# Kernel tuning notes

Measured on AMD Instinct MI355X. Metric: run time of the kernel, lower is better.

## Reference

```python
import jax, jax.numpy as jnp
import numpy as np

N, E = 50000, 400000
C_IN, C_OUT = 64, 32
K = 9  # kernel_size 3x3


def _quad_basis(t):
    # open B-spline basis, degree 2, per torch_spline_conv: k_mod in {0,1,2}
    # t = frac(pseudo * (kernel_size - degree)) = pseudo here (kernel_size=3, degree=2)
    return jnp.stack([0.5 * (1.0 - t) ** 2, -t * t + t + 0.5, 0.5 * t * t], axis=-1)  # [E,3]


def spline_basis(pseudo):
    # kernel_size=[3,3], degree=2, open spline: v = p*(3-2)=p, floor(v)=0 for p in [0,1),
    # so weight index for combination s is exactly s = k_mod0 + 3*k_mod1.
    q0 = _quad_basis(pseudo[:, 0])  # [E,3] varies with s%3
    q1 = _quad_basis(pseudo[:, 1])  # [E,3] varies with s//3
    return (q1[:, :, None] * q0[:, None, :]).reshape(-1, K)  # [E,9]


def spline_conv(x, src, dst, B, W, root, bias, n_nodes):
    xj = x[src]  # gather source node features [E,Cin]
    msg = jnp.zeros((xj.shape[0], W.shape[-1]), x.dtype)
    for k in range(K):  # fixed small kernel loop; avoids [E,K,Cin] blowup
        msg = msg + (xj * B[:, k, None]) @ W[k]
    agg = jax.ops.segment_sum(msg, dst, num_segments=n_nodes)  # aggr='add'
    return agg + x @ root + bias


def setup_inputs() -> dict:
    key = jax.random.key(0)
    ks = jax.random.split(key, 10)
    x = jax.random.normal(ks[0], (N, C_IN), jnp.float32)
    edge_index = jax.random.randint(ks[1], (2, E), 0, N, jnp.int64)
    pseudo = jax.random.uniform(ks[2], (E, 2), jnp.float32)
    skip = jax.random.normal(ks[3], (N, C_OUT), jnp.float32)
    s1 = 1.0 / np.sqrt(C_IN)
    s2 = 1.0 / np.sqrt(C_OUT)
    W1 = jax.random.normal(ks[4], (K, C_IN, C_OUT), jnp.float32) * s1
    root1 = jax.random.normal(ks[5], (C_IN, C_OUT), jnp.float32) * s1
    b1 = jnp.zeros((C_OUT,), jnp.float32)
    W2 = jax.random.normal(ks[6], (K, C_OUT, C_OUT), jnp.float32) * s2
    root2 = jax.random.normal(ks[7], (C_OUT, C_OUT), jnp.float32) * s2
    b2 = jnp.zeros((C_OUT,), jnp.float32)
    return {"x": x, "edge_index": edge_index, "pseudo": pseudo, "skip": skip,
            "W1": W1, "root1": root1, "b1": b1, "W2": W2, "root2": root2, "b2": b2}


def reference(x, edge_index, pseudo, skip, W1, root1, b1, W2, root2, b2):
    src, dst = edge_index[0], edge_index[1]  # flow: source_to_target
    B = spline_basis(pseudo)  # [E,9]
    n = x.shape[0]
    h = jax.nn.relu(spline_conv(x, src, dst, B, W1, root1, b1, n))
    h = jnp.concatenate([h, skip], axis=1)  # [N, Cout+Cskip] == [N, Cin]
    h = jax.nn.relu(spline_conv(h, src, dst, B, W1, root1, b1, n))
    h = jax.nn.relu(spline_conv(h, src, dst, B, W2, root2, b2, n))
    return h
```

## Files before the change

kernel.cpp:

```cpp
#include <hip/hip_runtime.h>
#include <hip/hip_bf16.h>


typedef __attribute__((ext_vector_type(8))) short short8;
typedef __attribute__((ext_vector_type(4))) float f32x4;

__device__ __forceinline__ float blo(unsigned u) {
    union { unsigned u; float f; } x; x.u = u << 16; return x.f;
}
__device__ __forceinline__ float bhi(unsigned u) {
    union { unsigned u; float f; } x; x.u = u & 0xffff0000u; return x.f;
}
__device__ __forceinline__ unsigned short f2bf(float f) {
    union { float f; unsigned u; } x; x.f = f;
    unsigned r = x.u + 0x7fffu + ((x.u >> 16) & 1u);
    return (unsigned short)(r >> 16);
}
__device__ __forceinline__ short8 cvt8(const float* p) {
    float4 a = *(const float4*)p;
    float4 b = *(const float4*)(p + 4);
    short8 r;
    r[0] = (short)f2bf(a.x); r[1] = (short)f2bf(a.y);
    r[2] = (short)f2bf(a.z); r[3] = (short)f2bf(a.w);
    r[4] = (short)f2bf(b.x); r[5] = (short)f2bf(b.y);
    r[6] = (short)f2bf(b.z); r[7] = (short)f2bf(b.w);
    return r;
}

#define YROW 296

__device__ __forceinline__ void m_phase(const unsigned short* sY,
                                        const int* __restrict__ sstart,
                                        const float4* __restrict__ erec,
                                        uint4* __restrict__ msgOut,
                                        int n0, int t, int N, int E)
{
    const int e0 = sstart[n0];
    const int e1 = (n0 + 32 < N) ? sstart[n0 + 32] : E;
    const int l  = t & 3;

    int e = e0 + (t >> 2);
    if (e >= e1) return;
    float4 r = erec[e];
    while (true) {
        const int en = e + 64;
        float4 rn;
        if (en < e1) rn = erec[en];

        const int srcl = __float_as_int(r.x) - n0;
        const int dp   = __float_as_int(r.y);
        const float p0 = r.z, p1 = r.w;

        const float qb[3] = {0.5f * (1.f - p0) * (1.f - p0), -p0 * p0 + p0 + 0.5f, 0.5f * p0 * p0};
        const float qa[3] = {0.5f * (1.f - p1) * (1.f - p1), -p1 * p1 + p1 + 0.5f, 0.5f * p1 * p1};

        const uint4* yb = (const uint4*)(sY + srcl * YROW) + l;
        float s[8] = {0.f, 0.f, 0.f, 0.f, 0.f, 0.f, 0.f, 0.f};
        #pragma unroll
        for (int a = 0; a < 3; ++a) {
            float z[8] = {0.f, 0.f, 0.f, 0.f, 0.f, 0.f, 0.f, 0.f};
            #pragma unroll
            for (int b = 0; b < 3; ++b) {
                uint4 v = yb[(a * 3 + b) * 4];
                const float cw = qb[b];
                z[0] = fmaf(cw, blo(v.x), z[0]); z[1] = fmaf(cw, bhi(v.x), z[1]);
                z[2] = fmaf(cw, blo(v.y), z[2]); z[3] = fmaf(cw, bhi(v.y), z[3]);
                z[4] = fmaf(cw, blo(v.z), z[4]); z[5] = fmaf(cw, bhi(v.z), z[5]);
                z[6] = fmaf(cw, blo(v.w), z[6]); z[7] = fmaf(cw, bhi(v.w), z[7]);
            }
            #pragma unroll
            for (int j = 0; j < 8; ++j) s[j] = fmaf(qa[a], z[j], s[j]);
        }

        union { uint4 u; __hip_bfloat162 h[4]; } o;
        #pragma unroll
        for (int j = 0; j < 4; ++j)
            o.h[j] = __float22bfloat162_rn(float2{s[2 * j], s[2 * j + 1]});
        msgOut[(size_t)dp * 4 + l] = o.u;

        if (en >= e1) break;
        r = rn; e = en;
    }
}

template<int NHALF>
__device__ __forceinline__ void t_core(short8 a0, short8 a1,
                                       const unsigned short* __restrict__ Wt,
                                       const float* __restrict__ bias,
                                       unsigned short* sY, float* __restrict__ aggOut,
                                       int n0, int rh, int cgp, int lc, int q, int N)
{
    const int CIN = NHALF * 32;
    #pragma unroll
    for (int j = 0; j < 10; ++j) {
        const int ti = cgp * 10 + j;
        const unsigned short* wp = Wt + ((size_t)(ti * 16 + lc)) * CIN + q * 8;
        f32x4 acc = (f32x4){0.f, 0.f, 0.f, 0.f};
        acc = __builtin_amdgcn_mfma_f32_16x16x32_bf16(a0, *(const short8*)wp, acc, 0, 0, 0);
        if (NHALF == 2)
            acc = __builtin_amdgcn_mfma_f32_16x16x32_bf16(a1, *(const short8*)(wp + 32), acc, 0, 0, 0);

        if (ti < 18) {
            #pragma unroll
            for (int r = 0; r < 4; ++r) {
                int nl = rh * 16 + q * 4 + r;
                sY[nl * YROW + ti * 16 + lc] = f2bf(acc[r]);
            }
        } else {
            int c = (ti - 18) * 16 + lc;
            float bv = bias[c];
            #pragma unroll
            for (int r = 0; r < 4; ++r) {
                int n = n0 + rh * 16 + q * 4 + r;
                if (n < N) aggOut[(size_t)n * 32 + c] = acc[r] + bv;
            }
        }
    }
}

__global__ __launch_bounds__(256, 8)
void layer_tm0(const float* __restrict__ Xa,
               const unsigned short* __restrict__ Wt, const float* __restrict__ bias,
               const int* __restrict__ sstart, const float4* __restrict__ erec,
               float* __restrict__ aggOut, uint4* __restrict__ msgOut, int N, int E)
{
    __shared__ __align__(16) unsigned short sY[32 * YROW];
    const int t = threadIdx.x, wv = t >> 6, lane = t & 63;
    const int lc = lane & 15, q = lane >> 4;
    const int rh = wv & 1, cgp = wv >> 1;
    const int n0 = blockIdx.x * 32;

    int na = n0 + rh * 16 + lc;
    if (na >= N) na = N - 1;
    const float* p = Xa + (size_t)na * 64 + q * 8;
    short8 a0 = cvt8(p);
    short8 a1 = cvt8(p + 32);

    t_core<2>(a0, a1, Wt, bias, sY, aggOut, n0, rh, cgp, lc, q, N);
    __syncthreads();
    m_phase(sY, sstart, erec, msgOut, n0, t, N, E);
}

template<int MODE>
__global__ __launch_bounds__(256, 8)
void layer_gtm(const float* __restrict__ aggPrev, const float* __restrict__ skipv,
               const unsigned short* __restrict__ Wt, const float* __restrict__ bias,
               const int* __restrict__ sstart, const int* __restrict__ dstart,
               const float4* __restrict__ erec,
               const uint4* __restrict__ msgIn, uint4* __restrict__ msgOut,
               float* __restrict__ aggOut, int N, int E)
{
    __shared__ __align__(16) unsigned short sY[32 * YROW];
    float* sH = (float*)sY;
    const int t = threadIdx.x, wv = t >> 6, lane = t & 63;
    const int lc = lane & 15, q = lane >> 4;
    const int rh = wv & 1, cgp = wv >> 1;
    const int n0 = blockIdx.x * 32;

    if (t < 128) {
        const int nl = t >> 2;
        const int l  = t & 3;
        int n = n0 + nl;
        if (n >= N) n = N - 1;
        const float* ap = aggPrev + (size_t)n * 32 + l * 8;
        float4 A = *(const float4*)ap;
        float4 B = *(const float4*)(ap + 4);
        float4 C = {0.f, 0.f, 0.f, 0.f}, D = {0.f, 0.f, 0.f, 0.f};
        const int e0 = dstart[n] - E;
        const int e1 = ((n + 1 < N) ? dstart[n + 1] : 2 * E) - E;
        const uint4* mp = msgIn + l;
        int e = e0;
        for (; e + 2 <= e1; e += 2) {
            uint4 v0 = mp[(size_t)e * 4];
            uint4 v1 = mp[(size_t)(e + 1) * 4];
            A.x += blo(v0.x); A.y += bhi(v0.x); A.z += blo(v0.y); A.w += bhi(v0.y);
            B.x += blo(v0.z); B.y += bhi(v0.z); B.z += blo(v0.w); B.w += bhi(v0.w);
            C.x += blo(v1.x); C.y += bhi(v1.x); C.z += blo(v1.y); C.w += bhi(v1.y);
            D.x += blo(v1.z); D.y += bhi(v1.z); D.z += blo(v1.w); D.w += bhi(v1.w);
        }
        if (e < e1) {
            uint4 v = mp[(size_t)e * 4];
            A.x += blo(v.x); A.y += bhi(v.x); A.z += blo(v.y); A.w += bhi(v.y);
            B.x += blo(v.z); B.y += bhi(v.z); B.z += blo(v.w); B.w += bhi(v.w);
        }
        float* hp = sH + nl * 33 + l * 8;
        hp[0] = fmaxf(A.x + C.x, 0.f); hp[1] = fmaxf(A.y + C.y, 0.f);
        hp[2] = fmaxf(A.z + C.z, 0.f); hp[3] = fmaxf(A.w + C.w, 0.f);
        hp[4] = fmaxf(B.x + D.x, 0.f); hp[5] = fmaxf(B.y + D.y, 0.f);
        hp[6] = fmaxf(B.z + D.z, 0.f); hp[7] = fmaxf(B.w + D.w, 0.f);
    }
    __syncthreads();

    const float* hp = sH + (rh * 16 + lc) * 33 + q * 8;
    union { short8 v; __hip_bfloat162 h2[4]; } pk;
    #pragma unroll
    for (int j = 0; j < 4; ++j)
        pk.h2[j] = __float22bfloat162_rn(float2{hp[2 * j], hp[2 * j + 1]});
    short8 a0 = pk.v;
    short8 a1;
    if (MODE == 1) {
        int na = n0 + rh * 16 + lc;
        if (na >= N) na = N - 1;
        a1 = cvt8(skipv + (size_t)na * 32 + q * 8);
    }
    __syncthreads();

    t_core<(MODE == 1) ? 2 : 1>(a0, a1, Wt, bias, sY, aggOut, n0, rh, cgp, lc, q, N);
    __syncthreads();
    m_phase(sY, sstart, erec, msgOut, n0, t, N, E);
}

__global__ __launch_bounds__(256)
void gather_kernel(const int* __restrict__ dstart, const uint4* __restrict__ msg4,
                   float* __restrict__ agg, int N, int E)
{
    const int t = threadIdx.x;
    const int n = blockIdx.x * 64 + (t >> 2);
    if (n >= N) return;
    const int l = t & 3;

    const int e0 = dstart[n] - E;
    const int e1 = ((n + 1 < N) ? dstart[n + 1] : 2 * E) - E;

    float4* ap = (float4*)(agg + (size_t)n * 32 + l * 8);
    float4 A = ap[0], B = ap[1];
    float4 C = {0.f, 0.f, 0.f, 0.f}, D = {0.f, 0.f, 0.f, 0.f};
    const uint4* mp = msg4 + l;
    int e = e0;
    for (; e + 2 <= e1; e += 2) {
        uint4 v0 = mp[(size_t)e * 4];
        uint4 v1 = mp[(size_t)(e + 1) * 4];
        A.x += blo(v0.x); A.y += bhi(v0.x); A.z += blo(v0.y); A.w += bhi(v0.y);
        B.x += blo(v0.z); B.y += bhi(v0.z); B.z += blo(v0.w); B.w += bhi(v0.w);
        C.x += blo(v1.x); C.y += bhi(v1.x); C.z += blo(v1.y); C.w += bhi(v1.y);
        D.x += blo(v1.z); D.y += bhi(v1.z); D.z += blo(v1.w); D.w += bhi(v1.w);
    }
    if (e < e1) {
        uint4 v = mp[(size_t)e * 4];
        A.x += blo(v.x); A.y += bhi(v.x); A.z += blo(v.y); A.w += bhi(v.y);
        B.x += blo(v.z); B.y += bhi(v.z); B.z += blo(v.w); B.w += bhi(v.w);
    }
    A.x += C.x; A.y += C.y; A.z += C.z; A.w += C.w;
    B.x += D.x; B.y += D.y; B.z += D.z; B.w += D.w;
    A.x = fmaxf(A.x, 0.f); A.y = fmaxf(A.y, 0.f); A.z = fmaxf(A.z, 0.f); A.w = fmaxf(A.w, 0.f);
    B.x = fmaxf(B.x, 0.f); B.y = fmaxf(B.y, 0.f); B.z = fmaxf(B.z, 0.f); B.w = fmaxf(B.w, 0.f);
    ap[0] = A; ap[1] = B;
}


__global__ __launch_bounds__(256)
void init_kernel(int* __restrict__ hist, int n2,
                 const float* __restrict__ W1, const float* __restrict__ root1,
                 const float* __restrict__ W2, const float* __restrict__ root2,
                 unsigned short* __restrict__ Wt1, unsigned short* __restrict__ Wt2)
{
    int i = blockIdx.x * 256 + threadIdx.x;
    if (i < n2) { hist[i] = 0; return; }
    int j = i - n2;
    if (j < 320 * 64) {
        int col = j / 64, k = j % 64;
        float v = (col < 288) ? W1[((size_t)(col >> 5) * 64 + k) * 32 + (col & 31)]
                              : root1[(size_t)k * 32 + (col - 288)];
        Wt1[j] = f2bf(v);
    } else if (j < 320 * 96) {
        int jj = j - 320 * 64;
        int col = jj / 32, k = jj % 32;
        float v = (col < 288) ? W2[((size_t)(col >> 5) * 32 + k) * 32 + (col & 31)]
                              : root2[(size_t)k * 32 + (col - 288)];
        Wt2[jj] = f2bf(v);
    }
}

__global__ __launch_bounds__(256)
void count_rank_kernel(const int* __restrict__ ei, int* __restrict__ hist,
                       uint2* __restrict__ rank, int N, int E)
{
    int e = blockIdx.x * 256 + threadIdx.x;
    if (e >= E) return;
    unsigned rs = atomicAdd((unsigned*)&hist[ei[e]], 1u);
    unsigned rd = atomicAdd((unsigned*)&hist[N + ei[E + e]], 1u);
    rank[e] = uint2{rs, rd};
}

__global__ __launch_bounds__(1024)
void scan1_kernel(int* __restrict__ hist, int* __restrict__ bsum, int n)
{
    __shared__ int s[1024];
    int tid = threadIdx.x;
    int i = blockIdx.x * 1024 + tid;
    int v = (i < n) ? hist[i] : 0;
    s[tid] = v;
    __syncthreads();
    for (int off = 1; off < 1024; off <<= 1) {
        int add = (tid >= off) ? s[tid - off] : 0;
        __syncthreads();
        s[tid] += add;
        __syncthreads();
    }
    if (i < n) hist[i] = s[tid] - v;
    if (tid == 1023) bsum[blockIdx.x] = s[1023];
}

__global__ __launch_bounds__(1024)
void scan3_kernel(int* __restrict__ hist, const int* __restrict__ bsum, int n)
{
    __shared__ int sred[128];
    int tid = threadIdx.x;
    int b = blockIdx.x;
    if (tid < 128) sred[tid] = (tid < b) ? bsum[tid] : 0;
    __syncthreads();
    for (int off = 64; off > 0; off >>= 1) {
        if (tid < off) sred[tid] += sred[tid + off];
        __syncthreads();
    }
    int pre = sred[0];
    int i = b * 1024 + tid;
    if (i < n) hist[i] += pre;
}

__global__ __launch_bounds__(256)
void scatter_plain_kernel(const int* __restrict__ ei, const float* __restrict__ pseudo,
                          const int* __restrict__ start, const uint2* __restrict__ rank,
                          float4* __restrict__ erec, int N, int E)
{
    int e = blockIdx.x * 256 + threadIdx.x;
    if (e >= E) return;
    int sv = ei[e];
    int dv = ei[E + e];
    uint2 rk = rank[e];
    int ps = start[sv] + (int)rk.x;
    int pd = start[N + dv] + (int)rk.y - E;
    float4 r;
    r.x = __int_as_float(sv);
    r.y = __int_as_float(pd);
    r.z = pseudo[2 * (size_t)e];
    r.w = pseudo[2 * (size_t)e + 1];
    erec[ps] = r;
}

extern "C" void kernel_launch(void* const* d_in, const int* in_sizes, int n_in,
                              void* d_out, int out_size, void* d_ws, size_t ws_size,
                              hipStream_t stream) {
    const float* x      = (const float*)d_in[0];
    const int*   ei     = (const int*)  d_in[1];
    const float* pseudo = (const float*)d_in[2];
    const float* skip   = (const float*)d_in[3];
    const float* W1     = (const float*)d_in[4];
    const float* root1  = (const float*)d_in[5];
    const float* b1     = (const float*)d_in[6];
    const float* W2     = (const float*)d_in[7];
    const float* root2  = (const float*)d_in[8];
    const float* b2     = (const float*)d_in[9];

    const int N = in_sizes[0] / 64;
    const int E = in_sizes[1] / 2;
    float* out = (float*)d_out;

    unsigned short* msgA = (unsigned short*)d_ws;
    unsigned short* msgB = msgA + (size_t)E * 32;
    float*  agg1  = (float*)(msgB + (size_t)E * 32);
    float*  agg2  = agg1 + (size_t)N * 32;
    float4* erec  = (float4*)(agg2 + (size_t)N * 32);
    int*    start = (int*)(erec + E);
    int*    bsum  = start + 2 * N;
    unsigned short* Wt1 = (unsigned short*)(bsum + 256);
    unsigned short* Wt2 = Wt1 + 320 * 64;
    uint2*  rank  = (uint2*)msgB;

    const dim3 blk(256);
    const int tb   = (N + 31) / 32;
    const int gb   = (N + 63) / 64;
    const int e256 = (E + 255) / 256;
    const int n2k  = (2 * N + 1023) / 1024;
    const int itot = 2 * N + 320 * 96;
    int* dstart = start + N;

    init_kernel<<<(itot + 255) / 256, blk, 0, stream>>>(start, 2 * N, W1, root1, W2, root2, Wt1, Wt2);
    count_rank_kernel<<<e256, blk, 0, stream>>>(ei, start, rank, N, E);
    scan1_kernel<<<n2k, 1024, 0, stream>>>(start, bsum, 2 * N);
    scan3_kernel<<<n2k, 1024, 0, stream>>>(start, bsum, 2 * N);
    scatter_plain_kernel<<<e256, blk, 0, stream>>>(ei, pseudo, start, rank, erec, N, E);

    layer_tm0<<<tb, blk, 0, stream>>>(x, Wt1, b1, start, erec, agg1, (uint4*)msgA, N, E);
    layer_gtm<1><<<tb, blk, 0, stream>>>(agg1, skip, Wt1, b1, start, dstart, erec,
                                         (const uint4*)msgA, (uint4*)msgB, agg2, N, E);
    layer_gtm<2><<<tb, blk, 0, stream>>>(agg2, nullptr, Wt2, b2, start, dstart, erec,
                                         (const uint4*)msgB, (uint4*)msgA, out, N, E);
    gather_kernel<<<gb, blk, 0, stream>>>(dstart, (const uint4*)msgA, out, N, E);
}
```

Measured before the change: 226.6 us.

## Split per-node edge gather across two thread halves and use nontemporal stores

```diff
diff --git a/kernel.cpp b/kernel.cpp
--- a/kernel.cpp
+++ b/kernel.cpp
@@ -4,6 +4,7 @@
 
 typedef __attribute__((ext_vector_type(8))) short short8;
 typedef __attribute__((ext_vector_type(4))) float f32x4;
+typedef __attribute__((ext_vector_type(4))) unsigned int u32x4;
 
 __device__ __forceinline__ float blo(unsigned u) {
     union { unsigned u; float f; } x; x.u = u << 16; return x.f;
@@ -72,11 +73,11 @@
             for (int j = 0; j < 8; ++j) s[j] = fmaf(qa[a], z[j], s[j]);
         }
 
-        union { uint4 u; __hip_bfloat162 h[4]; } o;
+        union { u32x4 u; __hip_bfloat162 h[4]; } o;
         #pragma unroll
         for (int j = 0; j < 4; ++j)
             o.h[j] = __float22bfloat162_rn(float2{s[2 * j], s[2 * j + 1]});
-        msgOut[(size_t)dp * 4 + l] = o.u;
+        __builtin_nontemporal_store(o.u, (u32x4*)&msgOut[(size_t)dp * 4 + l]);
 
         if (en >= e1) break;
         r = rn; e = en;
@@ -157,22 +158,29 @@
     const int rh = wv & 1, cgp = wv >> 1;
     const int n0 = blockIdx.x * 32;
 
-    if (t < 128) {
-        const int nl = t >> 2;
+    {
+        const int nl = t >> 3;
         const int l  = t & 3;
+        const int h  = (t >> 2) & 1;
         int n = n0 + nl;
         if (n >= N) n = N - 1;
-        const float* ap = aggPrev + (size_t)n * 32 + l * 8;
-        float4 A = *(const float4*)ap;
-        float4 B = *(const float4*)(ap + 4);
+        float4 A, B;
+        if (h == 0) {
+            const float* ap = aggPrev + (size_t)n * 32 + l * 8;
+            A = *(const float4*)ap;
+            B = *(const float4*)(ap + 4);
+        } else {
+            A = {0.f, 0.f, 0.f, 0.f};
+            B = {0.f, 0.f, 0.f, 0.f};
+        }
         float4 C = {0.f, 0.f, 0.f, 0.f}, D = {0.f, 0.f, 0.f, 0.f};
         const int e0 = dstart[n] - E;
         const int e1 = ((n + 1 < N) ? dstart[n + 1] : 2 * E) - E;
         const uint4* mp = msgIn + l;
-        int e = e0;
-        for (; e + 2 <= e1; e += 2) {
+        int e = e0 + h;
+        for (; e + 2 < e1; e += 4) {
             uint4 v0 = mp[(size_t)e * 4];
-            uint4 v1 = mp[(size_t)(e + 1) * 4];
+            uint4 v1 = mp[(size_t)(e + 2) * 4];
             A.x += blo(v0.x); A.y += bhi(v0.x); A.z += blo(v0.y); A.w += bhi(v0.y);
             B.x += blo(v0.z); B.y += bhi(v0.z); B.z += blo(v0.w); B.w += bhi(v0.w);
             C.x += blo(v1.x); C.y += bhi(v1.x); C.z += blo(v1.y); C.w += bhi(v1.y);
@@ -183,11 +191,19 @@
             A.x += blo(v.x); A.y += bhi(v.x); A.z += blo(v.y); A.w += bhi(v.y);
             B.x += blo(v.z); B.y += bhi(v.z); B.z += blo(v.w); B.w += bhi(v.w);
         }
-        float* hp = sH + nl * 33 + l * 8;
-        hp[0] = fmaxf(A.x + C.x, 0.f); hp[1] = fmaxf(A.y + C.y, 0.f);
-        hp[2] = fmaxf(A.z + C.z, 0.f); hp[3] = fmaxf(A.w + C.w, 0.f);
-        hp[4] = fmaxf(B.x + D.x, 0.f); hp[5] = fmaxf(B.y + D.y, 0.f);
-        hp[6] = fmaxf(B.z + D.z, 0.f); hp[7] = fmaxf(B.w + D.w, 0.f);
+        A.x += C.x; A.y += C.y; A.z += C.z; A.w += C.w;
+        B.x += D.x; B.y += D.y; B.z += D.z; B.w += D.w;
+        A.x += __shfl_xor(A.x, 4); A.y += __shfl_xor(A.y, 4);
+        A.z += __shfl_xor(A.z, 4); A.w += __shfl_xor(A.w, 4);
+        B.x += __shfl_xor(B.x, 4); B.y += __shfl_xor(B.y, 4);
+        B.z += __shfl_xor(B.z, 4); B.w += __shfl_xor(B.w, 4);
+        if (h == 0) {
+            float* hp = sH + nl * 33 + l * 8;
+            hp[0] = fmaxf(A.x, 0.f); hp[1] = fmaxf(A.y, 0.f);
+            hp[2] = fmaxf(A.z, 0.f); hp[3] = fmaxf(A.w, 0.f);
+            hp[4] = fmaxf(B.x, 0.f); hp[5] = fmaxf(B.y, 0.f);
+            hp[6] = fmaxf(B.z, 0.f); hp[7] = fmaxf(B.w, 0.f);
+        }
     }
     __syncthreads();
 
@@ -215,21 +231,24 @@
                    float* __restrict__ agg, int N, int E)
 {
     const int t = threadIdx.x;
-    const int n = blockIdx.x * 64 + (t >> 2);
+    const int n = blockIdx.x * 32 + (t >> 3);
     if (n >= N) return;
     const int l = t & 3;
+    const int h = (t >> 2) & 1;
 
     const int e0 = dstart[n] - E;
     const int e1 = ((n + 1 < N) ? dstart[n + 1] : 2 * E) - E;
 
     float4* ap = (float4*)(agg + (size_t)n * 32 + l * 8);
-    float4 A = ap[0], B = ap[1];
+    float4 A, B;
+    if (h == 0) { A = ap[0]; B = ap[1]; }
+    else { A = {0.f, 0.f, 0.f, 0.f}; B = {0.f, 0.f, 0.f, 0.f}; }
     float4 C = {0.f, 0.f, 0.f, 0.f}, D = {0.f, 0.f, 0.f, 0.f};
     const uint4* mp = msg4 + l;
-    int e = e0;
-    for (; e + 2 <= e1; e += 2) {
+    int e = e0 + h;
+    for (; e + 2 < e1; e += 4) {
         uint4 v0 = mp[(size_t)e * 4];
-        uint4 v1 = mp[(size_t)(e + 1) * 4];
+        uint4 v1 = mp[(size_t)(e + 2) * 4];
         A.x += blo(v0.x); A.y += bhi(v0.x); A.z += blo(v0.y); A.w += bhi(v0.y);
         B.x += blo(v0.z); B.y += bhi(v0.z); B.z += blo(v0.w); B.w += bhi(v0.w);
         C.x += blo(v1.x); C.y += bhi(v1.x); C.z += blo(v1.y); C.w += bhi(v1.y);
@@ -242,9 +261,15 @@
     }
     A.x += C.x; A.y += C.y; A.z += C.z; A.w += C.w;
     B.x += D.x; B.y += D.y; B.z += D.z; B.w += D.w;
-    A.x = fmaxf(A.x, 0.f); A.y = fmaxf(A.y, 0.f); A.z = fmaxf(A.z, 0.f); A.w = fmaxf(A.w, 0.f);
-    B.x = fmaxf(B.x, 0.f); B.y = fmaxf(B.y, 0.f); B.z = fmaxf(B.z, 0.f); B.w = fmaxf(B.w, 0.f);
-    ap[0] = A; ap[1] = B;
+    A.x += __shfl_xor(A.x, 4); A.y += __shfl_xor(A.y, 4);
+    A.z += __shfl_xor(A.z, 4); A.w += __shfl_xor(A.w, 4);
+    B.x += __shfl_xor(B.x, 4); B.y += __shfl_xor(B.y, 4);
+    B.z += __shfl_xor(B.z, 4); B.w += __shfl_xor(B.w, 4);
+    if (h == 0) {
+        A.x = fmaxf(A.x, 0.f); A.y = fmaxf(A.y, 0.f); A.z = fmaxf(A.z, 0.f); A.w = fmaxf(A.w, 0.f);
+        B.x = fmaxf(B.x, 0.f); B.y = fmaxf(B.y, 0.f); B.z = fmaxf(B.z, 0.f); B.w = fmaxf(B.w, 0.f);
+        ap[0] = A; ap[1] = B;
+    }
 }
 
 
@@ -330,12 +355,12 @@
     uint2 rk = rank[e];
     int ps = start[sv] + (int)rk.x;
     int pd = start[N + dv] + (int)rk.y - E;
-    float4 r;
-    r.x = __int_as_float(sv);
-    r.y = __int_as_float(pd);
-    r.z = pseudo[2 * (size_t)e];
-    r.w = pseudo[2 * (size_t)e + 1];
-    erec[ps] = r;
+    f32x4 r;
+    r[0] = __int_as_float(sv);
+    r[1] = __int_as_float(pd);
+    r[2] = pseudo[2 * (size_t)e];
+    r[3] = pseudo[2 * (size_t)e + 1];
+    __builtin_nontemporal_store(r, (f32x4*)&erec[ps]);
 }
 
 extern "C" void kernel_launch(void* const* d_in, const int* in_sizes, int n_in,
@@ -369,7 +394,7 @@
 
     const dim3 blk(256);
     const int tb   = (N + 31) / 32;
-    const int gb   = (N + 63) / 64;
+    const int gb   = (N + 31) / 32;
     const int e256 = (E + 255) / 256;
     const int n2k  = (2 * N + 1023) / 1024;
     const int itot = 2 * N + 320 * 96;
```

After: 390.2 us. 1.72x slower.

## Store edge messages in fp32 with 8 lanes per edge and two-edge pipelining

Applied to the files above, without the earlier changes.

```diff
diff --git a/kernel.cpp b/kernel.cpp
--- a/kernel.cpp
+++ b/kernel.cpp
@@ -29,57 +29,64 @@
 
 #define YROW 296
 
+__device__ __forceinline__ void m_edge(const unsigned short* sY, const float4 r,
+                                       float4* __restrict__ msgOut, int n0, int l)
+{
+    const int srcl = __float_as_int(r.x) - n0;
+    const int dp   = __float_as_int(r.y);
+    const float p0 = r.z, p1 = r.w;
+
+    const float qb[3] = {0.5f * (1.f - p0) * (1.f - p0), -p0 * p0 + p0 + 0.5f, 0.5f * p0 * p0};
+    const float qa[3] = {0.5f * (1.f - p1) * (1.f - p1), -p1 * p1 + p1 + 0.5f, 0.5f * p1 * p1};
+
+    const uint2* yb = (const uint2*)(sY + srcl * YROW) + l;
+    float s0 = 0.f, s1 = 0.f, s2 = 0.f, s3 = 0.f;
+    #pragma unroll
+    for (int a = 0; a < 3; ++a) {
+        float z0 = 0.f, z1 = 0.f, z2 = 0.f, z3 = 0.f;
+        #pragma unroll
+        for (int b = 0; b < 3; ++b) {
+            uint2 v = yb[(a * 3 + b) * 8];
+            const float cw = qb[b];
+            z0 = fmaf(cw, blo(v.x), z0); z1 = fmaf(cw, bhi(v.x), z1);
+            z2 = fmaf(cw, blo(v.y), z2); z3 = fmaf(cw, bhi(v.y), z3);
+        }
+        s0 = fmaf(qa[a], z0, s0); s1 = fmaf(qa[a], z1, s1);
+        s2 = fmaf(qa[a], z2, s2); s3 = fmaf(qa[a], z3, s3);
+    }
+    msgOut[(size_t)dp * 8 + l] = float4{s0, s1, s2, s3};
+}
+
 __device__ __forceinline__ void m_phase(const unsigned short* sY,
                                         const int* __restrict__ sstart,
                                         const float4* __restrict__ erec,
-                                        uint4* __restrict__ msgOut,
+                                        float4* __restrict__ msgOut,
                                         int n0, int t, int N, int E)
 {
     const int e0 = sstart[n0];
     const int e1 = (n0 + 32 < N) ? sstart[n0 + 32] : E;
-    const int l  = t & 3;
-
-    int e = e0 + (t >> 2);
+    const int l  = t & 7;
+
+    int e = e0 + (t >> 3);
     if (e >= e1) return;
-    float4 r = erec[e];
+    float4 r0 = erec[e];
+    bool  has1 = (e + 32 < e1);
+    float4 r1;
+    if (has1) r1 = erec[e + 32];
+
     while (true) {
-        const int en = e + 64;
-        float4 rn;
-        if (en < e1) rn = erec[en];
-
-        const int srcl = __float_as_int(r.x) - n0;
-        const int dp   = __float_as_int(r.y);
-        const float p0 = r.z, p1 = r.w;
-
-        const float qb[3] = {0.5f * (1.f - p0) * (1.f - p0), -p0 * p0 + p0 + 0.5f, 0.5f * p0 * p0};
-        const float qa[3] = {0.5f * (1.f - p1) * (1.f - p1), -p1 * p1 + p1 + 0.5f, 0.5f * p1 * p1};
-
-        const uint4* yb = (const uint4*)(sY + srcl * YROW) + l;
-        float s[8] = {0.f, 0.f, 0.f, 0.f, 0.f, 0.f, 0.f, 0.f};
-        #pragma unroll
-        for (int a = 0; a < 3; ++a) {
-            float z[8] = {0.f, 0.f, 0.f, 0.f, 0.f, 0.f, 0.f, 0.f};
-            #pragma unroll
-            for (int b = 0; b < 3; ++b) {
-                uint4 v = yb[(a * 3 + b) * 4];
-                const float cw = qb[b];
-                z[0] = fmaf(cw, blo(v.x), z[0]); z[1] = fmaf(cw, bhi(v.x), z[1]);
-                z[2] = fmaf(cw, blo(v.y), z[2]); z[3] = fmaf(cw, bhi(v.y), z[3]);
-                z[4] = fmaf(cw, blo(v.z), z[4]); z[5] = fmaf(cw, bhi(v.z), z[5]);
-                z[6] = fmaf(cw, blo(v.w), z[6]); z[7] = fmaf(cw, bhi(v.w), z[7]);
-            }
-            #pragma unroll
-            for (int j = 0; j < 8; ++j) s[j] = fmaf(qa[a], z[j], s[j]);
-        }
-
-        union { uint4 u; __hip_bfloat162 h[4]; } o;
-        #pragma unroll
-        for (int j = 0; j < 4; ++j)
-            o.h[j] = __float22bfloat162_rn(float2{s[2 * j], s[2 * j + 1]});
-        msgOut[(size_t)dp * 4 + l] = o.u;
-
-        if (en >= e1) break;
-        r = rn; e = en;
+        const int ep0 = e + 64, ep1 = e + 96;
+        const bool hp0 = ep0 < e1, hp1 = ep1 < e1;
+        float4 rp0, rp1;
+        if (hp0) rp0 = erec[ep0];
+        if (hp1) rp1 = erec[ep1];
+
+        m_edge(sY, r0, msgOut, n0, l);
+        if (!has1) break;
+        m_edge(sY, r1, msgOut, n0, l);
+
+        if (!hp0) break;
+        r0 = rp0; r1 = rp1; has1 = hp1; e = ep0;
     }
 }
 
@@ -118,11 +125,11 @@
     }
 }
 
-__global__ __launch_bounds__(256, 8)
+__global__ __launch_bounds__(256, 6)
 void layer_tm0(const float* __restrict__ Xa,
                const unsigned short* __restrict__ Wt, const float* __restrict__ bias,
                const int* __restrict__ sstart, const float4* __restrict__ erec,
-               float* __restrict__ aggOut, uint4* __restrict__ msgOut, int N, int E)
+               float* __restrict__ aggOut, float4* __restrict__ msgOut, int N, int E)
 {
     __shared__ __align__(16) unsigned short sY[32 * YROW];
     const int t = threadIdx.x, wv = t >> 6, lane = t & 63;
@@ -142,12 +149,12 @@
 }
 
 template<int MODE>
-__global__ __launch_bounds__(256, 8)
+__global__ __launch_bounds__(256, 6)
 void layer_gtm(const float* __restrict__ aggPrev, const float* __restrict__ skipv,
                const unsigned short* __restrict__ Wt, const float* __restrict__ bias,
                const int* __restrict__ sstart, const int* __restrict__ dstart,
                const float4* __restrict__ erec,
-               const uint4* __restrict__ msgIn, uint4* __restrict__ msgOut,
+               const float4* __restrict__ msgIn, float4* __restrict__ msgOut,
                float* __restrict__ aggOut, int N, int E)
 {
     __shared__ __align__(16) unsigned short sY[32 * YROW];
@@ -157,41 +164,36 @@
     const int rh = wv & 1, cgp = wv >> 1;
     const int n0 = blockIdx.x * 32;
 
-    if (t < 128) {
-        const int nl = t >> 2;
-        const int l  = t & 3;
+    {
+        const int nl = t >> 3;
+        const int j  = t & 7;
         int n = n0 + nl;
         if (n >= N) n = N - 1;
-        const float* ap = aggPrev + (size_t)n * 32 + l * 8;
-        float4 A = *(const float4*)ap;
-        float4 B = *(const float4*)(ap + 4);
-        float4 C = {0.f, 0.f, 0.f, 0.f}, D = {0.f, 0.f, 0.f, 0.f};
-        const int e0 = dstart[n] - E;
-        const int e1 = ((n + 1 < N) ? dstart[n + 1] : 2 * E) - E;
-        const uint4* mp = msgIn + l;
-        int e = e0;
-        for (; e + 2 <= e1; e += 2) {
-            uint4 v0 = mp[(size_t)e * 4];
-            uint4 v1 = mp[(size_t)(e + 1) * 4];
-            A.x += blo(v0.x); A.y += bhi(v0.x); A.z += blo(v0.y); A.w += bhi(v0.y);
-            B.x += blo(v0.z); B.y += bhi(v0.z); B.z += blo(v0.w); B.w += bhi(v0.w);
-            C.x += blo(v1.x); C.y += bhi(v1.x); C.z += blo(v1.y); C.w += bhi(v1.y);
-            D.x += blo(v1.z); D.y += bhi(v1.z); D.z += blo(v1.w); D.w += bhi(v1.w);
+        float4 A = *(const float4*)(aggPrev + (size_t)n * 32 + j * 4);
+        float4 C = {0.f, 0.f, 0.f, 0.f};
+        const int ge0 = dstart[n] - E;
+        const int ge1 = ((n + 1 < N) ? dstart[n + 1] : 2 * E) - E;
+        const float4* mp = msgIn + j;
+        int e = ge0;
+        for (; e + 1 < ge1; e += 2) {
+            float4 v0 = mp[(size_t)e * 8];
+            float4 v1 = mp[(size_t)(e + 1) * 8];
+            A.x += v0.x; A.y += v0.y; A.z += v0.z; A.w += v0.w;
+            C.x += v1.x; C.y += v1.y; C.z += v1.z; C.w += v1.w;
         }
-        if (e < e1) {
-            uint4 v = mp[(size_t)e * 4];
-            A.x += blo(v.x); A.y += bhi(v.x); A.z += blo(v.y); A.w += bhi(v.y);
-            B.x += blo(v.z); B.y += bhi(v.z); B.z += blo(v.w); B.w += bhi(v.w);
+        if (e < ge1) {
+            float4 v = mp[(size_t)e * 8];
+            A.x += v.x; A.y += v.y; A.z += v.z; A.w += v.w;
         }
-        float* hp = sH + nl * 33 + l * 8;
-        hp[0] = fmaxf(A.x + C.x, 0.f); hp[1] = fmaxf(A.y + C.y, 0.f);
-        hp[2] = fmaxf(A.z + C.z, 0.f); hp[3] = fmaxf(A.w + C.w, 0.f);
-        hp[4] = fmaxf(B.x + D.x, 0.f); hp[5] = fmaxf(B.y + D.y, 0.f);
-        hp[6] = fmaxf(B.z + D.z, 0.f); hp[7] = fmaxf(B.w + D.w, 0.f);
-    }
-    __syncthreads();
-
-    const float* hp = sH + (rh * 16 + lc) * 33 + q * 8;
+        A.x += C.x; A.y += C.y; A.z += C.z; A.w += C.w;
+        float4 R;
+        R.x = fmaxf(A.x, 0.f); R.y = fmaxf(A.y, 0.f);
+        R.z = fmaxf(A.z, 0.f); R.w = fmaxf(A.w, 0.f);
+        *(float4*)(sH + nl * 36 + j * 4) = R;
+    }
+    __syncthreads();
+
+    const float* hp = sH + (rh * 16 + lc) * 36 + q * 8;
     union { short8 v; __hip_bfloat162 h2[4]; } pk;
     #pragma unroll
     for (int j = 0; j < 4; ++j)
@@ -211,40 +213,36 @@
 }
 
 __global__ __launch_bounds__(256)
-void gather_kernel(const int* __restrict__ dstart, const uint4* __restrict__ msg4,
+void gather_kernel(const int* __restrict__ dstart, const float4* __restrict__ msg4,
                    float* __restrict__ agg, int N, int E)
 {
     const int t = threadIdx.x;
-    const int n = blockIdx.x * 64 + (t >> 2);
+    const int n = blockIdx.x * 32 + (t >> 3);
     if (n >= N) return;
-    const int l = t & 3;
+    const int j = t & 7;
 
     const int e0 = dstart[n] - E;
     const int e1 = ((n + 1 < N) ? dstart[n + 1] : 2 * E) - E;
 
-    float4* ap = (float4*)(agg + (size_t)n * 32 + l * 8);
-    float4 A = ap[0], B = ap[1];
-    float4 C = {0.f, 0.f, 0.f, 0.f}, D = {0.f, 0.f, 0.f, 0.f};
-    const uint4* mp = msg4 + l;
+    float4* ap = (float4*)(agg + (size_t)n * 32 + j * 4);
+    float4 A = ap[0];
+    float4 C = {0.f, 0.f, 0.f, 0.f};
+    const float4* mp = msg4 + j;
     int e = e0;
-    for (; e + 2 <= e1; e += 2) {
-        uint4 v0 = mp[(size_t)e * 4];
-        uint4 v1 = mp[(size_t)(e + 1) * 4];
-        A.x += blo(v0.x); A.y += bhi(v0.x); A.z += blo(v0.y); A.w += bhi(v0.y);
-        B.x += blo(v0.z); B.y += bhi(v0.z); B.z += blo(v0.w); B.w += bhi(v0.w);
-        C.x += blo(v1.x); C.y += bhi(v1.x); C.z += blo(v1.y); C.w += bhi(v1.y);
-        D.x += blo(v1.z); D.y += bhi(v1.z); D.z += blo(v1.w); D.w += bhi(v1.w);
+    for (; e + 1 < e1; e += 2) {
+        float4 v0 = mp[(size_t)e * 8];
+        float4 v1 = mp[(size_t)(e + 1) * 8];
+        A.x += v0.x; A.y += v0.y; A.z += v0.z; A.w += v0.w;
+        C.x += v1.x; C.y += v1.y; C.z += v1.z; C.w += v1.w;
     }
     if (e < e1) {
-        uint4 v = mp[(size_t)e * 4];
-        A.x += blo(v.x); A.y += bhi(v.x); A.z += blo(v.y); A.w += bhi(v.y);
-        B.x += blo(v.z); B.y += bhi(v.z); B.z += blo(v.w); B.w += bhi(v.w);
+        float4 v = mp[(size_t)e * 8];
+        A.x += v.x; A.y += v.y; A.z += v.z; A.w += v.w;
     }
     A.x += C.x; A.y += C.y; A.z += C.z; A.w += C.w;
-    B.x += D.x; B.y += D.y; B.z += D.z; B.w += D.w;
-    A.x = fmaxf(A.x, 0.f); A.y = fmaxf(A.y, 0.f); A.z = fmaxf(A.z, 0.f); A.w = fmaxf(A.w, 0.f);
-    B.x = fmaxf(B.x, 0.f); B.y = fmaxf(B.y, 0.f); B.z = fmaxf(B.z, 0.f); B.w = fmaxf(B.w, 0.f);
-    ap[0] = A; ap[1] = B;
+    A.x = fmaxf(A.x, 0.f); A.y = fmaxf(A.y, 0.f);
+    A.z = fmaxf(A.z, 0.f); A.w = fmaxf(A.w, 0.f);
+    ap[0] = A;
 }
 
 
@@ -356,9 +354,9 @@
     const int E = in_sizes[1] / 2;
     float* out = (float*)d_out;
 
-    unsigned short* msgA = (unsigned short*)d_ws;
-    unsigned short* msgB = msgA + (size_t)E * 32;
-    float*  agg1  = (float*)(msgB + (size_t)E * 32);
+    float*  msgA  = (float*)d_ws;
+    float*  msgB  = msgA + (size_t)E * 32;
+    float*  agg1  = msgB + (size_t)E * 32;
     float*  agg2  = agg1 + (size_t)N * 32;
     float4* erec  = (float4*)(agg2 + (size_t)N * 32);
     int*    start = (int*)(erec + E);
@@ -369,7 +367,7 @@
 
     const dim3 blk(256);
     const int tb   = (N + 31) / 32;
-    const int gb   = (N + 63) / 64;
+    const int gb   = (N + 31) / 32;
     const int e256 = (E + 255) / 256;
     const int n2k  = (2 * N + 1023) / 1024;
     const int itot = 2 * N + 320 * 96;
@@ -381,10 +379,10 @@
     scan3_kernel<<<n2k, 1024, 0, stream>>>(start, bsum, 2 * N);
     scatter_plain_kernel<<<e256, blk, 0, stream>>>(ei, pseudo, start, rank, erec, N, E);
 
-    layer_tm0<<<tb, blk, 0, stream>>>(x, Wt1, b1, start, erec, agg1, (uint4*)msgA, N, E);
+    layer_tm0<<<tb, blk, 0, stream>>>(x, Wt1, b1, start, erec, agg1, (float4*)msgA, N, E);
     layer_gtm<1><<<tb, blk, 0, stream>>>(agg1, skip, Wt1, b1, start, dstart, erec,
-                                         (const uint4*)msgA, (uint4*)msgB, agg2, N, E);
+                                         (const float4*)msgA, (float4*)msgB, agg2, N, E);
     layer_gtm<2><<<tb, blk, 0, stream>>>(agg2, nullptr, Wt2, b2, start, dstart, erec,
-                                         (const uint4*)msgB, (uint4*)msgA, out, N, E);
-    gather_kernel<<<gb, blk, 0, stream>>>(dstart, (const uint4*)msgA, out, N, E);
-}
+                                         (const float4*)msgB, (float4*)msgA, out, N, E);
+    gather_kernel<<<gb, blk, 0, stream>>>(dstart, (const float4*)msgA, out, N, E);
+}
```

New measurement: 242.0 us. +6.8%, slower.
